# Optimization experiments

Measured on AMD Instinct MI355X. Metric: run time of the kernel, lower is better.

The kernel has to match this reference:

```python
import jax, jax.numpy as jnp
import numpy as np

N_USER = 50000
N_ITEM = 50000
E = 600000
D = 128   # in_channels per node type
H = 128   # hidden_channels


def setup_inputs() -> dict:
    key = jax.random.key(0)
    ks = jax.random.split(key, 11)
    wscale = 1.0 / np.sqrt(D)  # stand-in for glorot
    inp = {
        "x_user": jax.random.normal(ks[0], (N_USER, D), jnp.float32),
        "x_item": jax.random.normal(ks[1], (N_ITEM, D), jnp.float32),
        "w_rates_src": jax.random.normal(ks[2], (D, H), jnp.float32) * wscale,
        "w_rates_tgt": jax.random.normal(ks[3], (D, H), jnp.float32) * wscale,
        "w_rated_src": jax.random.normal(ks[4], (D, H), jnp.float32) * wscale,
        "w_rated_tgt": jax.random.normal(ks[5], (D, H), jnp.float32) * wscale,
        "w_follows_src": jax.random.normal(ks[6], (D, H), jnp.float32) * wscale,
        "w_follows_tgt": jax.random.normal(ks[7], (D, H), jnp.float32) * wscale,
        "edge_rates": jax.random.randint(ks[8], (2, E), 0, N_ITEM, jnp.int32),
        "edge_rated": jax.random.randint(ks[9], (2, E), 0, N_USER, jnp.int32),
        "edge_follows": jax.random.randint(ks[10], (2, E), 0, N_USER, jnp.int32),
    }
    return inp


def _segment_mean(vals, idx, num_segments):
    # scatter(..., reduce='mean') into zeros: untouched rows stay 0
    s = jax.ops.segment_sum(vals, idx, num_segments=num_segments)
    cnt = jax.ops.segment_sum(jnp.ones((idx.shape[0], 1), vals.dtype), idx,
                              num_segments=num_segments)
    return s / jnp.maximum(cnt, 1.0)


def _relation(x_src, x_tgt, w_src, w_tgt, edges, n_tgt):
    src_x = x_src @ w_src                      # [N_src, H]
    tgt_x = x_tgt @ w_tgt                      # [N_tgt, H]
    msg = src_x[edges[0]]                      # gather  [E, H]
    agg = _segment_mean(msg, edges[1], n_tgt)  # scatter-mean [N_tgt, H]
    return tgt_x + agg


def reference(x_user, x_item, w_rates_src, w_rates_tgt, w_rated_src,
              w_rated_tgt, w_follows_src, w_follows_tgt, edge_rates,
              edge_rated, edge_follows):
    # ('user','rates','item') -> target item
    out_item = _relation(x_user, x_item, w_rates_src, w_rates_tgt,
                         edge_rates, N_ITEM)
    # ('item','rated_by','user') -> target user
    out_user = _relation(x_item, x_user, w_rated_src, w_rated_tgt,
                         edge_rated, N_USER)
    # ('user','follows','user') -> target user (accumulated)
    out_user = out_user + _relation(x_user, x_user, w_follows_src,
                                    w_follows_tgt, edge_follows, N_USER)
    # divide by number of relations per target type, then double relu
    out_user = jax.nn.relu(jax.nn.relu(out_user / 2.0))
    out_item = jax.nn.relu(jax.nn.relu(out_item / 1.0))
    return out_user, out_item
```

## Files before the change

### kernel.cpp

```cpp
#include <hip/hip_runtime.h>
#include <hip/hip_bf16.h>

constexpr int NN = 50000;
constexpr int DD = 128;
constexpr int EE = 600000;
constexpr long long PP = (long long)NN * DD;
constexpr int NE3 = 3 * EE;
constexpr int BW = 32;
constexpr int BPR = (NN + BW - 1) / BW;
constexpr int NBIN = 3 * BPR;
constexpr int NBR = 256;
constexpr int CHR = (EE + NBR - 1) / NBR;
constexpr int CAP = 1024;
constexpr float QSCALE = 4.0f / 127.0f;

typedef __bf16 bf16x8 __attribute__((ext_vector_type(8)));
typedef float f32x4 __attribute__((ext_vector_type(4)));

__device__ inline unsigned short f2bs(float x) {
    __hip_bfloat16 b = __float2bfloat16(x);
    return *reinterpret_cast<unsigned short*>(&b);
}
__device__ inline float bs2f(unsigned short u) {
    union { float f; unsigned int u; } x; x.u = ((unsigned int)u) << 16; return x.f;
}
__device__ inline unsigned char q8u(float x) {
    float c = fminf(fmaxf(x, -4.0f), 4.0f) * 31.75f;
    return (unsigned char)(__float2int_rn(c) + 128);
}

__global__ void cvtx_kernel(const float* __restrict__ xu, const float* __restrict__ xi,
                            unsigned short* __restrict__ xub, unsigned short* __restrict__ xib,
                            unsigned char* __restrict__ xu8, unsigned char* __restrict__ xi8) {
    const int total = (int)(PP / 4);
    for (int i = blockIdx.x * blockDim.x + threadIdx.x; i < total;
         i += gridDim.x * blockDim.x) {
        float4 a = ((const float4*)xu)[i];
        float4 b = ((const float4*)xi)[i];
        ushort4 oa, ob;
        oa.x = f2bs(a.x); oa.y = f2bs(a.y); oa.z = f2bs(a.z); oa.w = f2bs(a.w);
        ob.x = f2bs(b.x); ob.y = f2bs(b.y); ob.z = f2bs(b.z); ob.w = f2bs(b.w);
        ((ushort4*)xub)[i] = oa;
        ((ushort4*)xib)[i] = ob;
        uchar4 ca, cb;
        ca.x = q8u(a.x); ca.y = q8u(a.y); ca.z = q8u(a.z); ca.w = q8u(a.w);
        cb.x = q8u(b.x); cb.y = q8u(b.y); cb.z = q8u(b.z); cb.w = q8u(b.w);
        ((uchar4*)xu8)[i] = ca;
        ((uchar4*)xi8)[i] = cb;
    }
}

__global__ void wprep_kernel(const float* __restrict__ wrt, const float* __restrict__ wft,
                             const float* __restrict__ wrs, const float* __restrict__ wfs,
                             const float* __restrict__ wit, const float* __restrict__ wis,
                             unsigned short* __restrict__ Wu, unsigned short* __restrict__ Wi) {
    int n = blockIdx.x;
    for (int k = threadIdx.x; k < 384; k += blockDim.x) {
        int seg = k >> 7, ks = k & 127;
        float v = (seg == 0) ? (wrt[ks * 128 + n] + wft[ks * 128 + n])
                : (seg == 1) ? wrs[ks * 128 + n] : wfs[ks * 128 + n];
        Wu[n * 384 + k] = f2bs(v);
    }
    for (int k = threadIdx.x; k < 256; k += blockDim.x) {
        int seg = k >> 7, ks = k & 127;
        float v = (seg == 0) ? wit[ks * 128 + n] : wis[ks * 128 + n];
        Wi[n * 256 + k] = f2bs(v);
    }
}


__global__ __launch_bounds__(256) void bucket_hist_kernel(
    const int* __restrict__ t0, const int* __restrict__ t1,
    const int* __restrict__ t2, unsigned int* __restrict__ hist) {
    __shared__ unsigned int h[BPR];
    const int rel = blockIdx.y;
    const int* tp = (rel == 0) ? t0 : (rel == 1) ? t1 : t2;
    for (int i = threadIdx.x; i < BPR; i += 256) h[i] = 0;
    __syncthreads();
    const int start = blockIdx.x * CHR;
    const int end = (start + CHR < EE) ? start + CHR : EE;
    for (int e = start + threadIdx.x; e < end; e += 256)
        atomicAdd(&h[tp[e] >> 5], 1u);
    __syncthreads();
    unsigned int* out = hist + ((size_t)rel * NBR + blockIdx.x) * BPR;
    for (int i = threadIdx.x; i < BPR; i += 256) out[i] = h[i];
}

__global__ void bucket_base_kernel(const unsigned int* __restrict__ hist,
                                   unsigned int* __restrict__ base,
                                   unsigned int* __restrict__ bintot) {
    int bin = blockIdx.x * blockDim.x + threadIdx.x;
    if (bin >= NBIN) return;
    int rel = bin / BPR, bl = bin - rel * BPR;
    unsigned int run = 0;
    for (int b = 0; b < NBR; ++b) {
        size_t idx = ((size_t)rel * NBR + b) * BPR + bl;
        unsigned int v = hist[idx];
        base[idx] = run;
        run += v;
    }
    bintot[bin] = run;
}

__global__ __launch_bounds__(256) void scan_part_kernel(
    const int* __restrict__ cnt, int* __restrict__ rowst,
    int* __restrict__ bsum, int n) {
    const int tid = threadIdx.x;
    const int base = tid * 20;
    int v[20];
    #pragma unroll
    for (int i = 0; i < 20; ++i) {
        int g = base + i;
        v[i] = (g < n) ? cnt[g] : 0;
    }
    int s = 0;
    #pragma unroll
    for (int i = 0; i < 20; ++i) s += v[i];
    const int lane = tid & 63, wv = tid >> 6;
    int incl = s;
    #pragma unroll
    for (int d = 1; d < 64; d <<= 1) {
        int u = __shfl_up(incl, d, 64);
        if (lane >= d) incl += u;
    }
    __shared__ int wsum[4];
    if (lane == 63) wsum[wv] = incl;
    __syncthreads();
    int woff = 0;
    for (int w = 0; w < wv; ++w) woff += wsum[w];
    int run = woff + incl - s;
    #pragma unroll
    for (int i = 0; i < 20; ++i) {
        int g = base + i;
        if (g < n) rowst[g] = run;
        run += v[i];
    }
    if (tid == 255) bsum[0] = woff + incl;
}

__global__ __launch_bounds__(256) void bucket_scatter_kernel(
    const int* __restrict__ s0, const int* __restrict__ t0,
    const int* __restrict__ s1, const int* __restrict__ t1,
    const int* __restrict__ s2, const int* __restrict__ t2,
    const unsigned int* __restrict__ base, const int* __restrict__ bkstart,
    unsigned int* __restrict__ bucketed) {
    __shared__ unsigned int cur[BPR];
    const int rel = blockIdx.y;
    const int* tp = (rel == 0) ? t0 : (rel == 1) ? t1 : t2;
    const int* sp = (rel == 0) ? s0 : (rel == 1) ? s1 : s2;
    const unsigned int* bb = base + ((size_t)rel * NBR + blockIdx.x) * BPR;
    const int* bks = bkstart + rel * BPR;
    for (int i = threadIdx.x; i < BPR; i += 256)
        cur[i] = (unsigned int)bks[i] + bb[i];
    __syncthreads();
    const int start = blockIdx.x * CHR;
    const int end = (start + CHR < EE) ? start + CHR : EE;
    for (int e = start + threadIdx.x; e < end; e += 256) {
        int t = tp[e];
        unsigned int pos = atomicAdd(&cur[t >> 5], 1u);
        bucketed[pos] = ((unsigned int)(t & 31) << 16) | (unsigned int)sp[e];
    }
}

__global__ __launch_bounds__(256) void bucket_gather_kernel(
    const unsigned char* __restrict__ xu8, const unsigned char* __restrict__ xi8,
    const int* __restrict__ bkstart, const unsigned int* __restrict__ bucketed,
    unsigned short* __restrict__ accb) {
    __shared__ unsigned int raw[CAP];
    __shared__ unsigned short sorted[CAP];
    __shared__ unsigned int fcnt[BW], fstart[BW], cursor[BW];

    const int b = blockIdx.x;
    const int rel = b / BPR;
    const int tb = (b - rel * BPR) * BW;
    const unsigned char* srcm = (rel == 0) ? xi8 : xu8;
    const int start = bkstart[b];
    const int end = (b == NBIN - 1) ? NE3 : bkstart[b + 1];

    const int tid = threadIdx.x;
    const int grp = tid >> 4;
    const int l = tid & 15;

    unsigned int s[2][4];
    int deg[2] = {0, 0};
    #pragma unroll
    for (int q = 0; q < 2; ++q)
        #pragma unroll
        for (int k = 0; k < 4; ++k) s[q][k] = 0u;

    for (int c0 = start; c0 < end; c0 += CAP) {
        const int n = (end - c0 < CAP) ? end - c0 : CAP;
        if (tid < BW) fcnt[tid] = 0;
        __syncthreads();
        for (int i = tid; i < n; i += 256) {
            unsigned int r = bucketed[c0 + i];
            raw[i] = r;
            atomicAdd(&fcnt[r >> 16], 1u);
        }
        __syncthreads();
        if (tid < BW) {
            unsigned int v = fcnt[tid];
            unsigned int incl = v;
            #pragma unroll
            for (int d = 1; d < BW; d <<= 1) {
                unsigned int u = __shfl_up(incl, d, 64);
                if ((tid & 63) >= d) incl += u;
            }
            fstart[tid] = incl - v;
            cursor[tid] = incl - v;
        }
        __syncthreads();
        for (int i = tid; i < n; i += 256) {
            unsigned int r = raw[i];
            unsigned int pos = atomicAdd(&cursor[r >> 16], 1u);
            sorted[pos] = (unsigned short)r;
        }
        __syncthreads();

        #pragma unroll
        for (int q = 0; q < 2; ++q) {
            const int f = grp + 16 * q;
            const int cf = (int)fcnt[f];
            const int st = (int)fstart[f];
            deg[q] += cf;
            int j = 0;
            for (; j + 4 <= cf; j += 4) {
                int sa = sorted[st + j];
                int sb = sorted[st + j + 1];
                int sc = sorted[st + j + 2];
                int sd = sorted[st + j + 3];
                uint2 va = *(const uint2*)(srcm + (size_t)sa * DD + l * 8);
                uint2 vb = *(const uint2*)(srcm + (size_t)sb * DD + l * 8);
                uint2 vc = *(const uint2*)(srcm + (size_t)sc * DD + l * 8);
                uint2 vd = *(const uint2*)(srcm + (size_t)sd * DD + l * 8);
                s[q][0] += (va.x & 0x00FF00FFu) + (vb.x & 0x00FF00FFu)
                         + (vc.x & 0x00FF00FFu) + (vd.x & 0x00FF00FFu);
                s[q][1] += ((va.x >> 8) & 0x00FF00FFu) + ((vb.x >> 8) & 0x00FF00FFu)
                         + ((vc.x >> 8) & 0x00FF00FFu) + ((vd.x >> 8) & 0x00FF00FFu);
                s[q][2] += (va.y & 0x00FF00FFu) + (vb.y & 0x00FF00FFu)
                         + (vc.y & 0x00FF00FFu) + (vd.y & 0x00FF00FFu);
                s[q][3] += ((va.y >> 8) & 0x00FF00FFu) + ((vb.y >> 8) & 0x00FF00FFu)
                         + ((vc.y >> 8) & 0x00FF00FFu) + ((vd.y >> 8) & 0x00FF00FFu);
            }
            for (; j < cf; ++j) {
                int sa = sorted[st + j];
                uint2 va = *(const uint2*)(srcm + (size_t)sa * DD + l * 8);
                s[q][0] += (va.x & 0x00FF00FFu);
                s[q][1] += ((va.x >> 8) & 0x00FF00FFu);
                s[q][2] += (va.y & 0x00FF00FFu);
                s[q][3] += ((va.y >> 8) & 0x00FF00FFu);
            }
        }
        __syncthreads();
    }

    #pragma unroll
    for (int q = 0; q < 2; ++q) {
        const int f = grp + 16 * q;
        const int t = tb + f;
        if (t < NN) {
            float bias = 128.0f * (float)deg[q];
            float inv = QSCALE / (float)(deg[q] > 1 ? deg[q] : 1);
            float m[8];
            m[0] = ((float)(s[q][0] & 0xFFFFu) - bias) * inv;
            m[2] = ((float)(s[q][0] >> 16)    - bias) * inv;
            m[1] = ((float)(s[q][1] & 0xFFFFu) - bias) * inv;
            m[3] = ((float)(s[q][1] >> 16)    - bias) * inv;
            m[4] = ((float)(s[q][2] & 0xFFFFu) - bias) * inv;
            m[6] = ((float)(s[q][2] >> 16)    - bias) * inv;
            m[5] = ((float)(s[q][3] & 0xFFFFu) - bias) * inv;
            m[7] = ((float)(s[q][3] >> 16)    - bias) * inv;
            uint4 o;
            o.x = ((unsigned int)f2bs(m[1]) << 16) | f2bs(m[0]);
            o.y = ((unsigned int)f2bs(m[3]) << 16) | f2bs(m[2]);
            o.z = ((unsigned int)f2bs(m[5]) << 16) | f2bs(m[4]);
            o.w = ((unsigned int)f2bs(m[7]) << 16) | f2bs(m[6]);
            *(uint4*)(accb + (size_t)(rel * NN + t) * DD + l * 8) = o;
        }
    }
}

template<int KSTEPS>
__device__ __forceinline__ void gemm_body(
    const unsigned short* __restrict__ a0, const unsigned short* __restrict__ a1,
    const unsigned short* __restrict__ a2, const unsigned short* __restrict__ Wt,
    float* __restrict__ outp, float postmul,
    unsigned char* lAb, unsigned char* lBb) {
    const int tid = threadIdx.x;
    const int m0 = blockIdx.x * 128;
    const int Ktot = KSTEPS * 64;
    const int wv = tid >> 6, lane = tid & 63;

    f32x4 acc[2][8];
    #pragma unroll
    for (int i = 0; i < 2; ++i)
        #pragma unroll
        for (int j = 0; j < 8; ++j) acc[i][j] = (f32x4)(0.f);

    int rowA[4], cgA[4];
    #pragma unroll
    for (int i = 0; i < 4; ++i) {
        int o = (wv * 4 + i) * 1024 + lane * 16;
        rowA[i] = o >> 7;
        cgA[i] = ((o >> 4) & 7) ^ (rowA[i] & 7);
    }

    for (int kt = 0; kt < KSTEPS; ++kt) {
        const unsigned short* As = (kt >> 1) == 0 ? a0 : (kt >> 1) == 1 ? a1 : a2;
        const int ks0 = (kt & 1) * 64;
        #pragma unroll
        for (int i = 0; i < 4; ++i) {
            const unsigned short* src =
                As + (size_t)(m0 + rowA[i]) * DD + ks0 + cgA[i] * 8;
            __builtin_amdgcn_global_load_lds(
                (const __attribute__((address_space(1))) void*)src,
                (__attribute__((address_space(3))) void*)(lAb + (wv * 4 + i) * 1024),
                16, 0, 0);
        }
        #pragma unroll
        for (int i = 0; i < 4; ++i) {
            const unsigned short* src =
                Wt + (size_t)rowA[i] * Ktot + kt * 64 + cgA[i] * 8;
            __builtin_amdgcn_global_load_lds(
                (const __attribute__((address_space(1))) void*)src,
                (__attribute__((address_space(3))) void*)(lBb + (wv * 4 + i) * 1024),
                16, 0, 0);
        }
        __syncthreads();

        #pragma unroll
        for (int kk = 0; kk < 2; ++kk) {
            bf16x8 af[2];
            #pragma unroll
            for (int mi = 0; mi < 2; ++mi) {
                int row = wv * 32 + mi * 16 + (lane & 15);
                int byte = (row * 128 + kk * 64 + (lane >> 4) * 16) ^ ((row & 7) << 4);
                af[mi] = *(const bf16x8*)(lAb + byte);
            }
            #pragma unroll
            for (int ni = 0; ni < 8; ++ni) {
                int n = ni * 16 + (lane & 15);
                int byte = (n * 128 + kk * 64 + (lane >> 4) * 16) ^ ((n & 7) << 4);
                bf16x8 bfr = *(const bf16x8*)(lBb + byte);
                acc[0][ni] = __builtin_amdgcn_mfma_f32_16x16x32_bf16(
                    af[0], bfr, acc[0][ni], 0, 0, 0);
                acc[1][ni] = __builtin_amdgcn_mfma_f32_16x16x32_bf16(
                    af[1], bfr, acc[1][ni], 0, 0, 0);
            }
        }
        __syncthreads();
    }

    #pragma unroll
    for (int mi = 0; mi < 2; ++mi) {
        #pragma unroll
        for (int ni = 0; ni < 8; ++ni) {
            #pragma unroll
            for (int r = 0; r < 4; ++r) {
                int g = m0 + wv * 32 + mi * 16 + (lane >> 4) * 4 + r;
                if (g < NN) {
                    float v = acc[mi][ni][r] * postmul;
                    outp[(size_t)g * DD + ni * 16 + (lane & 15)] = v > 0.f ? v : 0.f;
                }
            }
        }
    }
}

__global__ __launch_bounds__(256) void mfma_gemm2_kernel(
    const unsigned short* __restrict__ xub, const unsigned short* __restrict__ xib,
    const unsigned short* __restrict__ accb, const unsigned short* __restrict__ Wu,
    const unsigned short* __restrict__ Wi, float* __restrict__ out_user,
    float* __restrict__ out_item) {
    __shared__ unsigned char lAb[128 * 128];
    __shared__ unsigned char lBb[128 * 128];
    if (blockIdx.y == 0)
        gemm_body<6>(xub, accb, accb + PP, Wu, out_user, 0.5f, lAb, lBb);
    else
        gemm_body<4>(xib, accb + 2 * PP, nullptr, Wi, out_item, 1.0f, lAb, lBb);
}

extern "C" void kernel_launch(void* const* d_in, const int* in_sizes, int n_in,
                              void* d_out, int out_size, void* d_ws, size_t ws_size,
                              hipStream_t stream) {
    const float* x_user = (const float*)d_in[0];
    const float* x_item = (const float*)d_in[1];
    const float* w_rates_src   = (const float*)d_in[2];
    const float* w_rates_tgt   = (const float*)d_in[3];
    const float* w_rated_src   = (const float*)d_in[4];
    const float* w_rated_tgt   = (const float*)d_in[5];
    const float* w_follows_src = (const float*)d_in[6];
    const float* w_follows_tgt = (const float*)d_in[7];
    const int* e_rates   = (const int*)d_in[8];
    const int* e_rated   = (const int*)d_in[9];
    const int* e_follows = (const int*)d_in[10];

    char* p = (char*)d_ws;
    unsigned short* xub  = (unsigned short*)p; p += (size_t)PP * 2;
    unsigned short* xib  = (unsigned short*)p; p += (size_t)PP * 2;
    unsigned char* xu8   = (unsigned char*)p; p += (size_t)PP;
    unsigned char* xi8   = (unsigned char*)p; p += (size_t)PP;
    unsigned short* accb = (unsigned short*)p; p += (size_t)3 * PP * 2;
    unsigned short* Wu   = (unsigned short*)p; p += (size_t)128 * 384 * 2;
    unsigned short* Wi   = (unsigned short*)p; p += (size_t)128 * 256 * 2;
    unsigned int* bintot = (unsigned int*)p; p += (size_t)NBIN * 4;
    int* bkstart         = (int*)p; p += (size_t)(NBIN + 64) * 4;
    int* bsum            = (int*)p; p += (size_t)64 * 4;
    unsigned int* bucketed = (unsigned int*)p; p += (size_t)NE3 * 4;

    unsigned int* hist = (unsigned int*)accb;
    unsigned int* base = hist + (size_t)3 * NBR * BPR;

    float* out_user = (float*)d_out;
    float* out_item = out_user + PP;

    cvtx_kernel<<<2048, 256, 0, stream>>>(x_user, x_item, xub, xib, xu8, xi8);
    wprep_kernel<<<128, 256, 0, stream>>>(w_rated_tgt, w_follows_tgt, w_rated_src,
                                          w_follows_src, w_rates_tgt, w_rates_src,
                                          Wu, Wi);
    dim3 gh(NBR, 3);
    bucket_hist_kernel<<<gh, 256, 0, stream>>>(e_rated + EE, e_follows + EE,
                                               e_rates + EE, hist);
    bucket_base_kernel<<<(NBIN + 255) / 256, 256, 0, stream>>>(hist, base, bintot);
    scan_part_kernel<<<1, 256, 0, stream>>>((const int*)bintot, bkstart, bsum, NBIN);
    bucket_scatter_kernel<<<gh, 256, 0, stream>>>(e_rated, e_rated + EE,
                                                  e_follows, e_follows + EE,
                                                  e_rates, e_rates + EE,
                                                  base, bkstart, bucketed);
    bucket_gather_kernel<<<NBIN, 256, 0, stream>>>(xu8, xi8, bkstart, bucketed, accb);

    dim3 gg((NN + 127) / 128, 2);
    mfma_gemm2_kernel<<<gg, 256, 0, stream>>>(xub, xib, accb, Wu, Wi,
                                              out_user, out_item);
}
```

Before: 140.2 us.

## Halve histogram chunks and split bucket scatter into bin slices per block

The histogram now uses 128 edge chunks instead of 256, which halves the per-chunk histogram storage and the serial prefix loop in bucket_base. The scatter kernel launches eight blocks per chunk, each owning one slice of bins with a much smaller shared cursor array. Each block still reads every edge in its chunk and skips targets outside its slice. This trades eight times the edge-index reads for higher occupancy and less cursor initialisation per block, while keeping the output order deterministic within each bin.

New measurement: 131.7 us, median of 2. 6.0% less time.

```diff
diff --git a/kernel.cpp b/kernel.cpp
--- a/kernel.cpp
+++ b/kernel.cpp
@@ -9,8 +9,10 @@
 constexpr int BW = 32;
 constexpr int BPR = (NN + BW - 1) / BW;
 constexpr int NBIN = 3 * BPR;
-constexpr int NBR = 256;
-constexpr int CHR = (EE + NBR - 1) / NBR;
+constexpr int NCHK = 128;
+constexpr int CH2 = (EE + NCHK - 1) / NCHK;
+constexpr int NSL = 8;
+constexpr int SLW = (BPR + NSL - 1) / NSL;
 constexpr int CAP = 1024;
 constexpr float QSCALE = 4.0f / 127.0f;
 
@@ -77,12 +79,12 @@
     const int* tp = (rel == 0) ? t0 : (rel == 1) ? t1 : t2;
     for (int i = threadIdx.x; i < BPR; i += 256) h[i] = 0;
     __syncthreads();
-    const int start = blockIdx.x * CHR;
-    const int end = (start + CHR < EE) ? start + CHR : EE;
+    const int start = blockIdx.x * CH2;
+    const int end = (start + CH2 < EE) ? start + CH2 : EE;
     for (int e = start + threadIdx.x; e < end; e += 256)
         atomicAdd(&h[tp[e] >> 5], 1u);
     __syncthreads();
-    unsigned int* out = hist + ((size_t)rel * NBR + blockIdx.x) * BPR;
+    unsigned int* out = hist + ((size_t)rel * NCHK + blockIdx.x) * BPR;
     for (int i = threadIdx.x; i < BPR; i += 256) out[i] = h[i];
 }
 
@@ -93,8 +95,8 @@
     if (bin >= NBIN) return;
     int rel = bin / BPR, bl = bin - rel * BPR;
     unsigned int run = 0;
-    for (int b = 0; b < NBR; ++b) {
-        size_t idx = ((size_t)rel * NBR + b) * BPR + bl;
+    for (int b = 0; b < NCHK; ++b) {
+        size_t idx = ((size_t)rel * NCHK + b) * BPR + bl;
         unsigned int v = hist[idx];
         base[idx] = run;
         run += v;
@@ -144,20 +146,26 @@
     const int* __restrict__ s2, const int* __restrict__ t2,
     const unsigned int* __restrict__ base, const int* __restrict__ bkstart,
     unsigned int* __restrict__ bucketed) {
-    __shared__ unsigned int cur[BPR];
+    __shared__ unsigned int cur[SLW];
     const int rel = blockIdx.y;
+    const int chunk = blockIdx.x >> 3;
+    const int sl = blockIdx.x & 7;
+    const int b0 = sl * SLW;
+    const int b1 = (b0 + SLW < BPR) ? b0 + SLW : BPR;
     const int* tp = (rel == 0) ? t0 : (rel == 1) ? t1 : t2;
     const int* sp = (rel == 0) ? s0 : (rel == 1) ? s1 : s2;
-    const unsigned int* bb = base + ((size_t)rel * NBR + blockIdx.x) * BPR;
+    const unsigned int* bb = base + ((size_t)rel * NCHK + chunk) * BPR;
     const int* bks = bkstart + rel * BPR;
-    for (int i = threadIdx.x; i < BPR; i += 256)
-        cur[i] = (unsigned int)bks[i] + bb[i];
+    for (int i = threadIdx.x; i < b1 - b0; i += 256)
+        cur[i] = (unsigned int)bks[b0 + i] + bb[b0 + i];
     __syncthreads();
-    const int start = blockIdx.x * CHR;
-    const int end = (start + CHR < EE) ? start + CHR : EE;
+    const int start = chunk * CH2;
+    const int end = (start + CH2 < EE) ? start + CH2 : EE;
     for (int e = start + threadIdx.x; e < end; e += 256) {
         int t = tp[e];
-        unsigned int pos = atomicAdd(&cur[t >> 5], 1u);
+        int bin = t >> 5;
+        if (bin < b0 || bin >= b1) continue;
+        unsigned int pos = atomicAdd(&cur[bin - b0], 1u);
         bucketed[pos] = ((unsigned int)(t & 31) << 16) | (unsigned int)sp[e];
     }
 }
@@ -409,7 +417,7 @@
     unsigned int* bucketed = (unsigned int*)p; p += (size_t)NE3 * 4;
 
     unsigned int* hist = (unsigned int*)accb;
-    unsigned int* base = hist + (size_t)3 * NBR * BPR;
+    unsigned int* base = hist + (size_t)3 * NCHK * BPR;
 
     float* out_user = (float*)d_out;
     float* out_item = out_user + PP;
@@ -418,12 +426,13 @@
     wprep_kernel<<<128, 256, 0, stream>>>(w_rated_tgt, w_follows_tgt, w_rated_src,
                                           w_follows_src, w_rates_tgt, w_rates_src,
                                           Wu, Wi);
-    dim3 gh(NBR, 3);
+    dim3 gh(NCHK, 3);
     bucket_hist_kernel<<<gh, 256, 0, stream>>>(e_rated + EE, e_follows + EE,
                                                e_rates + EE, hist);
     bucket_base_kernel<<<(NBIN + 255) / 256, 256, 0, stream>>>(hist, base, bintot);
     scan_part_kernel<<<1, 256, 0, stream>>>((const int*)bintot, bkstart, bsum, NBIN);
-    bucket_scatter_kernel<<<gh, 256, 0, stream>>>(e_rated, e_rated + EE,
+    dim3 gs(NCHK * NSL, 3);
+    bucket_scatter_kernel<<<gs, 256, 0, stream>>>(e_rated, e_rated + EE,
                                                   e_follows, e_follows + EE,
                                                   e_rates, e_rates + EE,
                                                   base, bkstart, bucketed);
```
